# Kernel optimization log

Hardware: AMD Instinct MI355X
Metric: run time of the kernel (lower is better)

## Reference

```python
import jax, jax.numpy as jnp
import numpy as np

D_MODEL = 1024
N_HEADS = 16
HEAD_DIM = D_MODEL // N_HEADS
BATCH = 4
SEQ = 2048


def setup_inputs() -> dict:
    key = jax.random.key(0)
    ks = jax.random.split(key, 5)
    # Xavier uniform bound for square d_model x d_model weights
    bound = np.sqrt(6.0 / (D_MODEL + D_MODEL))
    x = jax.random.normal(ks[0], (BATCH, SEQ, D_MODEL), dtype=jnp.float32)
    attention_mask = jnp.ones((BATCH, SEQ), dtype=jnp.int32)
    wq = jax.random.uniform(ks[1], (D_MODEL, D_MODEL), jnp.float32, -bound, bound)
    wk = jax.random.uniform(ks[2], (D_MODEL, D_MODEL), jnp.float32, -bound, bound)
    wv = jax.random.uniform(ks[3], (D_MODEL, D_MODEL), jnp.float32, -bound, bound)
    wo = jax.random.uniform(ks[4], (D_MODEL, D_MODEL), jnp.float32, -bound, bound)
    return {"x": x, "attention_mask": attention_mask,
            "wq": wq, "wk": wk, "wv": wv, "wo": wo}


def reference(x, attention_mask, wq, wk, wv, wo):
    # x: (B, S, D). Linear weights stored torch-style (out, in): y = x @ W^T
    B, S, D = x.shape
    H, Hd = N_HEADS, HEAD_DIM
    scale = np.sqrt(Hd).astype(np.float32)

    def split_heads(t):  # (B,S,D) -> (B,H,S,Hd)
        return t.reshape(B, S, H, Hd).transpose(0, 2, 1, 3)

    q = split_heads(jnp.einsum('bsd,ed->bse', x, wq))
    k = split_heads(jnp.einsum('bsd,ed->bse', x, wk))
    v = split_heads(jnp.einsum('bsd,ed->bse', x, wv))

    scores = jnp.einsum('bhqd,bhkd->bhqk', q, k) / scale  # (B,H,S,S)

    causal = jnp.tril(jnp.ones((S, S), dtype=bool))  # True = keep
    keep = causal[None, None, :, :] & (attention_mask[:, None, None, :] != 0)
    scores = jnp.where(keep, scores, -jnp.inf)

    attn = jax.nn.softmax(scores, axis=-1)  # dropout: eval mode (identity)
    out = jnp.einsum('bhqk,bhkd->bhqd', attn, v)  # (B,H,S,Hd)
    out = out.transpose(0, 2, 1, 3).reshape(B, S, D)
    return jnp.einsum('bsd,ed->bse', out, wo)
```

## Files before the change

kernel.cpp:

```cpp
#include <hip/hip_runtime.h>
#include <cstdint>
#include <cstddef>

#define D_MODEL 1024
#define N_HEADS 16
#define HEAD_DIM 64
#define BATCH 4
#define SEQ 2048
#define M_TOTAL (BATCH * SEQ)

typedef __attribute__((ext_vector_type(8))) short bf16x8;
typedef __attribute__((ext_vector_type(4))) float f32x4;
typedef __attribute__((ext_vector_type(16))) float f32x16;

#define Q_SCALE 0.18033688011112042f

__device__ __forceinline__ unsigned short f2bu(float f) {
    union { float f; unsigned u; } x; x.f = f;
    unsigned r = x.u + 0x7FFFu + ((x.u >> 16) & 1u);
    return (unsigned short)(r >> 16);
}
__device__ __forceinline__ unsigned short f2bu_fast(float f) {
    union { float f; unsigned u; } x; x.f = f;
    return (unsigned short)((x.u + 0x8000u) >> 16);
}

__device__ __forceinline__ void async16(void* lds, const void* g) {
    __builtin_amdgcn_global_load_lds(
        (const __attribute__((address_space(1))) void*)g,
        (__attribute__((address_space(3))) void*)lds, 16, 0, 0);
}

__global__ __launch_bounds__(256) void cast_all(const float* __restrict__ x,
                                                const float* __restrict__ wq,
                                                const float* __restrict__ wk,
                                                const float* __restrict__ wv,
                                                const float* __restrict__ wo,
                                                unsigned short* __restrict__ dst) {
    const size_t NE = (size_t)M_TOTAL * D_MODEL;
    const size_t WE = (size_t)D_MODEL * D_MODEL;
    size_t i4 = (size_t)blockIdx.x * 256 + threadIdx.x;
    size_t e = i4 * 4;
    const float* src; size_t off;
    if (e < NE) { src = x; off = e; }
    else {
        size_t t = e - NE;
        int r = (int)(t / WE); off = t - (size_t)r * WE;
        src = (r == 0) ? wq : (r == 1) ? wk : (r == 2) ? wv : wo;
    }
    float4 v = *(const float4*)(src + off);
    ushort4 o;
    o.x = f2bu(v.x); o.y = f2bu(v.y); o.z = f2bu(v.z); o.w = f2bu(v.w);
    ((ushort4*)dst)[i4] = o;
}

__global__ __launch_bounds__(256) void qkv_gemm(const unsigned short* __restrict__ X,
                                                const unsigned short* __restrict__ W0,
                                                const unsigned short* __restrict__ W1,
                                                const unsigned short* __restrict__ W2,
                                                unsigned short* __restrict__ Y0,
                                                unsigned short* __restrict__ Y1,
                                                unsigned short* __restrict__ Vt) {
    __shared__ short As[128 * 32];
    __shared__ short Bs[128 * 32];

    const int sel = blockIdx.x >> 3;
    const unsigned short* W = (sel == 0) ? W0 : (sel == 1) ? W1 : W2;
    const float scl = (sel == 0) ? Q_SCALE : 1.0f;

    const int tid = threadIdx.x;
    const int w = tid >> 6, lane = tid & 63, quad = lane >> 4, l15 = lane & 15;
    const int wm = w & 1, wn = w >> 1;
    const int rowBase = blockIdx.y * 128;
    const int colBase = (blockIdx.x & 7) * 128;

    f32x4 acc[4][4];
#pragma unroll
    for (int mi = 0; mi < 4; ++mi)
#pragma unroll
        for (int ni = 0; ni < 4; ++ni)
#pragma unroll
            for (int e = 0; e < 4; ++e) acc[mi][ni][e] = 0.f;

    for (int k0 = 0; k0 < 1024; k0 += 32) {
        __syncthreads();
#pragma unroll
        for (int l = 0; l < 2; ++l) {
            int c = tid + l * 256;
            int row = c >> 2, ccs = c & 3;
            int cc = ccs ^ ((row >> 1) & 3);
            async16((char*)As + c * 16, X + (size_t)(rowBase + row) * 1024 + k0 + cc * 8);
            async16((char*)Bs + c * 16, W + (size_t)(colBase + row) * 1024 + k0 + cc * 8);
        }
        __syncthreads();

        bf16x8 a[4], b[4];
#pragma unroll
        for (int mi = 0; mi < 4; ++mi) {
            int r = wm * 64 + mi * 16 + l15;
            int slot = quad ^ ((r >> 1) & 3);
            a[mi] = *(const bf16x8*)&As[r * 32 + slot * 8];
        }
#pragma unroll
        for (int ni = 0; ni < 4; ++ni) {
            int r = wn * 64 + ni * 16 + l15;
            int slot = quad ^ ((r >> 1) & 3);
            b[ni] = *(const bf16x8*)&Bs[r * 32 + slot * 8];
        }
#pragma unroll
        for (int mi = 0; mi < 4; ++mi)
#pragma unroll
            for (int ni = 0; ni < 4; ++ni)
                acc[mi][ni] = __builtin_amdgcn_mfma_f32_16x16x32_bf16(a[mi], b[ni], acc[mi][ni], 0, 0, 0);
    }

    if (sel != 2) {
        unsigned short* Y = (sel == 0) ? Y0 : Y1;
#pragma unroll
        for (int mi = 0; mi < 4; ++mi)
#pragma unroll
            for (int ni = 0; ni < 4; ++ni)
#pragma unroll
                for (int reg = 0; reg < 4; ++reg) {
                    int row = rowBase + wm * 64 + mi * 16 + quad * 4 + reg;
                    int col = colBase + wn * 64 + ni * 16 + l15;
                    Y[(size_t)row * 1024 + col] = f2bu(acc[mi][ni][reg] * scl);
                }
    } else {
#pragma unroll
        for (int mi = 0; mi < 4; ++mi) {
            int row0 = rowBase + wm * 64 + mi * 16 + quad * 4;
            int bb = row0 >> 11;
            int s0 = row0 & 2047;
#pragma unroll
            for (int ni = 0; ni < 4; ++ni) {
                int col = colBase + wn * 64 + ni * 16 + l15;
                int hh = col >> 6, dd = col & 63;
                ushort4 pk;
                pk.x = f2bu(acc[mi][ni][0]); pk.y = f2bu(acc[mi][ni][1]);
                pk.z = f2bu(acc[mi][ni][2]); pk.w = f2bu(acc[mi][ni][3]);
                *(ushort4*)(Vt + (((size_t)bb * 16 + hh) * 64 + dd) * SEQ + s0) = pk;
            }
        }
    }
}

__global__ __launch_bounds__(256) void out_gemm(const unsigned short* __restrict__ X,
                                                const unsigned short* __restrict__ W,
                                                float* __restrict__ Y) {
    __shared__ short As[128 * 32];
    __shared__ short Bs[128 * 32];

    const int tid = threadIdx.x;
    const int w = tid >> 6, lane = tid & 63, quad = lane >> 4, l15 = lane & 15;
    const int wm = w & 1, wn = w >> 1;
    const int rowBase = blockIdx.y * 128;
    const int colBase = blockIdx.x * 128;

    f32x4 acc[4][4];
#pragma unroll
    for (int mi = 0; mi < 4; ++mi)
#pragma unroll
        for (int ni = 0; ni < 4; ++ni)
#pragma unroll
            for (int e = 0; e < 4; ++e) acc[mi][ni][e] = 0.f;

    for (int k0 = 0; k0 < 1024; k0 += 32) {
        __syncthreads();
#pragma unroll
        for (int l = 0; l < 2; ++l) {
            int c = tid + l * 256;
            int row = c >> 2, ccs = c & 3;
            int cc = ccs ^ ((row >> 1) & 3);
            async16((char*)As + c * 16, X + (size_t)(rowBase + row) * 1024 + k0 + cc * 8);
            async16((char*)Bs + c * 16, W + (size_t)(colBase + row) * 1024 + k0 + cc * 8);
        }
        __syncthreads();

        bf16x8 a[4], b[4];
#pragma unroll
        for (int mi = 0; mi < 4; ++mi) {
            int r = wm * 64 + mi * 16 + l15;
            int slot = quad ^ ((r >> 1) & 3);
            a[mi] = *(const bf16x8*)&As[r * 32 + slot * 8];
        }
#pragma unroll
        for (int ni = 0; ni < 4; ++ni) {
            int r = wn * 64 + ni * 16 + l15;
            int slot = quad ^ ((r >> 1) & 3);
            b[ni] = *(const bf16x8*)&Bs[r * 32 + slot * 8];
        }
#pragma unroll
        for (int mi = 0; mi < 4; ++mi)
#pragma unroll
            for (int ni = 0; ni < 4; ++ni)
                acc[mi][ni] = __builtin_amdgcn_mfma_f32_16x16x32_bf16(a[mi], b[ni], acc[mi][ni], 0, 0, 0);
    }

#pragma unroll
    for (int mi = 0; mi < 4; ++mi)
#pragma unroll
        for (int ni = 0; ni < 4; ++ni)
#pragma unroll
            for (int reg = 0; reg < 4; ++reg) {
                int row = rowBase + wm * 64 + mi * 16 + quad * 4 + reg;
                int col = colBase + wn * 64 + ni * 16 + l15;
                Y[(size_t)row * 1024 + col] = acc[mi][ni][reg];
            }
}

__global__ __launch_bounds__(256) void flash32(const unsigned short* __restrict__ Q,
                                               const unsigned short* __restrict__ K,
                                               const unsigned short* __restrict__ Vt,
                                               const int* __restrict__ mask,
                                               unsigned short* __restrict__ CTX) {
    __shared__ short lds[9216];
    __shared__ float biasS[64];
    __shared__ int allokS;

    short* Ks = lds;
    short* Vs = lds + 4096;

    const int pid = blockIdx.x;
    const int bh = blockIdx.y;
    const int b = bh >> 4;
    const int tid = threadIdx.x;
    const int w = tid >> 6, lane = tid & 63, l31 = lane & 31, lane5 = lane >> 5;

    const size_t qkBase = (size_t)b * SEQ * D_MODEL + (size_t)(bh & 15) * HEAD_DIM;
    const size_t vtBase = (size_t)bh * HEAD_DIM * SEQ;

    int stp[2], stcc[2], stj[2];
#pragma unroll
    for (int l = 0; l < 2; ++l) {
        int c = tid + l * 256;
        int p = c >> 3, sl = c & 7;
        stp[l] = p;
        stcc[l] = sl ^ (p & 7);
        stj[l] = (p & 0x33) | ((p & 4) << 1) | ((p & 8) >> 1);
    }

    for (int phase = 0; phase < 2; ++phase) {
        const int qt = phase ? pid : 15 - pid;
        const int q0 = qt * 128;
        const int iq = q0 + w * 32 + l31;

        bf16x8 qf[4];
#pragma unroll
        for (int ks = 0; ks < 4; ++ks)
            qf[ks] = *(const bf16x8*)(Q + qkBase + (size_t)iq * D_MODEL + ks * 16 + lane5 * 8);

        float mv = -INFINITY, lv = 0.f;
        f32x16 Ot[2];
#pragma unroll
        for (int dt = 0; dt < 2; ++dt)
#pragma unroll
            for (int e = 0; e < 16; ++e) Ot[dt][e] = 0.f;

        const int ktmax = 2 * qt + 1;

        uint4 kreg[2], vreg[2];
        int mreg;
        {
            const int k0 = 0;
#pragma unroll
            for (int l = 0; l < 2; ++l) {
                kreg[l] = *(const uint4*)(K + qkBase + (size_t)(k0 + stj[l]) * D_MODEL + stcc[l] * 8);
                vreg[l] = *(const uint4*)(Vt + vtBase + (size_t)stp[l] * SEQ + k0 + stcc[l] * 8);
            }
            mreg = (tid < 64) ? mask[b * SEQ + k0 + tid] : 1;
        }

        for (int kt = 0; kt <= ktmax; ++kt) {
            const int k0 = kt * 64;
            __syncthreads();
#pragma unroll
            for (int l = 0; l < 2; ++l) {
                int c = tid + l * 256;
                *(uint4*)((char*)Ks + c * 16) = kreg[l];
                *(uint4*)((char*)Vs + c * 16) = vreg[l];
            }
            if (tid < 64) {
                biasS[tid] = mreg ? 0.f : -INFINITY;
                unsigned long long bal = __ballot(mreg != 0);
                if (tid == 0) allokS = (bal == ~0ull) ? 1 : 0;
            }
            if (kt < ktmax) {
                const int kn = k0 + 64;
#pragma unroll
                for (int l = 0; l < 2; ++l) {
                    kreg[l] = *(const uint4*)(K + qkBase + (size_t)(kn + stj[l]) * D_MODEL + stcc[l] * 8);
                    vreg[l] = *(const uint4*)(Vt + vtBase + (size_t)stp[l] * SEQ + kn + stcc[l] * 8);
                }
                mreg = (tid < 64) ? mask[b * SEQ + kn + tid] : 1;
            }
            __syncthreads();

            if (64 * kt > q0 + 32 * w + 31) continue;

            f32x16 St[2];
#pragma unroll
            for (int T = 0; T < 2; ++T)
#pragma unroll
                for (int e = 0; e < 16; ++e) St[T][e] = 0.f;
#pragma unroll
            for (int T = 0; T < 2; ++T)
#pragma unroll
                for (int ks = 0; ks < 4; ++ks) {
                    int p = T * 32 + l31;
                    int slot = (ks * 2 + lane5) ^ (p & 7);
                    bf16x8 a = *(const bf16x8*)&Ks[p * 64 + slot * 8];
                    St[T] = __builtin_amdgcn_mfma_f32_32x32x16_bf16(a, qf[ks], St[T], 0, 0, 0);
                }

            const bool partial = (k0 + 63 > q0 + 32 * w);
            if (partial) {
#pragma unroll
                for (int T = 0; T < 2; ++T)
#pragma unroll
                    for (int r = 0; r < 16; ++r) {
                        int j = k0 + 32 * T + 16 * (r >> 3) + 8 * lane5 + (r & 7);
                        if (j > iq) St[T][r] = -INFINITY;
                    }
            }
            if (!allokS) {
#pragma unroll
                for (int T = 0; T < 2; ++T)
#pragma unroll
                    for (int r = 0; r < 16; ++r)
                        St[T][r] += biasS[32 * T + 16 * (r >> 3) + 8 * lane5 + (r & 7)];
            }

            float rm = -INFINITY;
#pragma unroll
            for (int T = 0; T < 2; ++T)
#pragma unroll
                for (int r = 0; r < 16; ++r) rm = fmaxf(rm, St[T][r]);
            rm = fmaxf(rm, __shfl_xor(rm, 32));
            float mn = fmaxf(mv, rm);
            float al = (mv > -INFINITY) ? exp2f(mv - mn) : 0.f;
            float rs = 0.f;
#pragma unroll
            for (int T = 0; T < 2; ++T)
#pragma unroll
                for (int r = 0; r < 16; ++r) {
                    float pv = (St[T][r] > -INFINITY) ? exp2f(St[T][r] - mn) : 0.f;
                    St[T][r] = pv;
                    rs += pv;
                }
            rs += __shfl_xor(rs, 32);
            lv = lv * al + rs;
            mv = mn;
#pragma unroll
            for (int dt = 0; dt < 2; ++dt)
#pragma unroll
                for (int e = 0; e < 16; ++e) Ot[dt][e] *= al;

            bf16x8 pf[4];
#pragma unroll
            for (int t = 0; t < 4; ++t) {
                int T = t >> 1, hb = t & 1;
#pragma unroll
                for (int jj = 0; jj < 8; ++jj)
                    pf[t][jj] = (short)f2bu_fast(St[T][hb * 8 + jj]);
            }

#pragma unroll
            for (int dt = 0; dt < 2; ++dt)
#pragma unroll
                for (int t = 0; t < 4; ++t) {
                    int p = dt * 32 + l31;
                    int slot = (t * 2 + lane5) ^ (p & 7);
                    bf16x8 a = *(const bf16x8*)&Vs[p * 64 + slot * 8];
                    Ot[dt] = __builtin_amdgcn_mfma_f32_32x32x16_bf16(a, pf[t], Ot[dt], 0, 0, 0);
                }
        }

        __syncthreads();
        const float inv = 1.f / lv;
#pragma unroll
        for (int dt = 0; dt < 2; ++dt)
#pragma unroll
            for (int k = 0; k < 8; ++k) {
                int r0 = 2 * k;
                int d = (r0 & 3) + 4 * lane5 + 8 * (r0 >> 2) + 32 * dt;
                unsigned lo = f2bu(Ot[dt][r0] * inv);
                unsigned hi = f2bu(Ot[dt][r0 + 1] * inv);
                *(unsigned*)&lds[(w * 32 + l31) * 72 + d] = lo | (hi << 16);
            }
        __syncthreads();
#pragma unroll
        for (int k = 0; k < 4; ++k) {
            int id = tid + k * 256;
            int r = id >> 3, cc = id & 7;
            uint4 v = *(const uint4*)&lds[r * 72 + cc * 8];
            *(uint4*)(CTX + qkBase + (size_t)(q0 + r) * D_MODEL + cc * 8) = v;
        }
    }
}

extern "C" void kernel_launch(void* const* d_in, const int* in_sizes, int n_in,
                              void* d_out, int out_size, void* d_ws, size_t ws_size,
                              hipStream_t stream) {
    const float* x  = (const float*)d_in[0];
    const int* mask = (const int*)d_in[1];
    const float* wq = (const float*)d_in[2];
    const float* wk = (const float*)d_in[3];
    const float* wv = (const float*)d_in[4];
    const float* wo = (const float*)d_in[5];
    float* out = (float*)d_out;

    const size_t NE = (size_t)M_TOTAL * D_MODEL;
    const size_t WE = (size_t)D_MODEL * D_MODEL;
    unsigned short* ws  = (unsigned short*)d_ws;
    unsigned short* xb  = ws;
    unsigned short* wqb = xb + NE;
    unsigned short* wkb = wqb + WE;
    unsigned short* wvb = wkb + WE;
    unsigned short* wob = wvb + WE;
    unsigned short* Qb  = wob + WE;
    unsigned short* Kb  = Qb + NE;
    unsigned short* Vtb = Kb + NE;
    unsigned short* CTX = Vtb + NE;

    cast_all<<<(int)((NE + 4 * WE) / 4 / 256), 256, 0, stream>>>(x, wq, wk, wv, wo, ws);

    qkv_gemm<<<dim3(24, M_TOTAL / 128), 256, 0, stream>>>(xb, wqb, wkb, wvb, Qb, Kb, Vtb);

    flash32<<<dim3(8, BATCH * N_HEADS), 256, 0, stream>>>(Qb, Kb, Vtb, mask, CTX);

    out_gemm<<<dim3(D_MODEL / 128, M_TOTAL / 128), 256, 0, stream>>>(CTX, wob, out);
}
```

Measured before the change: 315.6 us.

## Skip per-tile mask work, lazily rescale softmax, use packed bf16 cvt and setprio

Each block now checks the whole padding mask once up front and skips the per-tile mask loads, ballots and bias adds when every key is valid. The online softmax only rescales O and l when the running max rises by more than 8 (log2 units), which removes most rescale multiplies. The exp2 guards are dropped and the per-element bf16 packing is replaced with hardware v_cvt_pk_bf16_f32. MFMA sections are wrapped in s_setprio. Risks: the lazy rescale lets P values reach up to 2^8 before conversion to bf16, and the extra full-mask scan adds a prologue pass per block.

After: 309.3 us. 2.0% less time.

```diff
diff --git a/kernel.cpp b/kernel.cpp
--- a/kernel.cpp
+++ b/kernel.cpp
@@ -19,10 +19,6 @@
     union { float f; unsigned u; } x; x.f = f;
     unsigned r = x.u + 0x7FFFu + ((x.u >> 16) & 1u);
     return (unsigned short)(r >> 16);
-}
-__device__ __forceinline__ unsigned short f2bu_fast(float f) {
-    union { float f; unsigned u; } x; x.f = f;
-    return (unsigned short)((x.u + 0x8000u) >> 16);
 }
 
 __device__ __forceinline__ void async16(void* lds, const void* g) {
@@ -217,6 +213,7 @@
     __shared__ short lds[9216];
     __shared__ float biasS[64];
     __shared__ int allokS;
+    __shared__ int okW[4];
 
     short* Ks = lds;
     short* Vs = lds + 4096;
@@ -229,6 +226,15 @@
 
     const size_t qkBase = (size_t)b * SEQ * D_MODEL + (size_t)(bh & 15) * HEAD_DIM;
     const size_t vtBase = (size_t)bh * HEAD_DIM * SEQ;
+
+    {
+        int ok = 1;
+        for (int i = tid; i < SEQ; i += 256) ok &= (mask[b * SEQ + i] != 0);
+        unsigned long long bal = __ballot(ok != 0);
+        if (lane == 0) okW[w] = (bal == ~0ull) ? 1 : 0;
+    }
+    __syncthreads();
+    const int allSeq = okW[0] & okW[1] & okW[2] & okW[3];
 
     int stp[2], stcc[2], stj[2];
 #pragma unroll
@@ -260,7 +266,7 @@
         const int ktmax = 2 * qt + 1;
 
         uint4 kreg[2], vreg[2];
-        int mreg;
+        int mreg = 1;
         {
             const int k0 = 0;
 #pragma unroll
@@ -268,7 +274,7 @@
                 kreg[l] = *(const uint4*)(K + qkBase + (size_t)(k0 + stj[l]) * D_MODEL + stcc[l] * 8);
                 vreg[l] = *(const uint4*)(Vt + vtBase + (size_t)stp[l] * SEQ + k0 + stcc[l] * 8);
             }
-            mreg = (tid < 64) ? mask[b * SEQ + k0 + tid] : 1;
+            if (!allSeq && tid < 64) mreg = mask[b * SEQ + k0 + tid];
         }
 
         for (int kt = 0; kt <= ktmax; ++kt) {
@@ -280,7 +286,7 @@
                 *(uint4*)((char*)Ks + c * 16) = kreg[l];
                 *(uint4*)((char*)Vs + c * 16) = vreg[l];
             }
-            if (tid < 64) {
+            if (!allSeq && tid < 64) {
                 biasS[tid] = mreg ? 0.f : -INFINITY;
                 unsigned long long bal = __ballot(mreg != 0);
                 if (tid == 0) allokS = (bal == ~0ull) ? 1 : 0;
@@ -292,7 +298,7 @@
                     kreg[l] = *(const uint4*)(K + qkBase + (size_t)(kn + stj[l]) * D_MODEL + stcc[l] * 8);
                     vreg[l] = *(const uint4*)(Vt + vtBase + (size_t)stp[l] * SEQ + kn + stcc[l] * 8);
                 }
-                mreg = (tid < 64) ? mask[b * SEQ + kn + tid] : 1;
+                if (!allSeq && tid < 64) mreg = mask[b * SEQ + kn + tid];
             }
             __syncthreads();
 
@@ -303,6 +309,7 @@
             for (int T = 0; T < 2; ++T)
 #pragma unroll
                 for (int e = 0; e < 16; ++e) St[T][e] = 0.f;
+            __builtin_amdgcn_s_setprio(1);
 #pragma unroll
             for (int T = 0; T < 2; ++T)
 #pragma unroll
@@ -312,6 +319,7 @@
                     bf16x8 a = *(const bf16x8*)&Ks[p * 64 + slot * 8];
                     St[T] = __builtin_amdgcn_mfma_f32_32x32x16_bf16(a, qf[ks], St[T], 0, 0, 0);
                 }
+            __builtin_amdgcn_s_setprio(0);
 
             const bool partial = (k0 + 63 > q0 + 32 * w);
             if (partial) {
@@ -323,7 +331,7 @@
                         if (j > iq) St[T][r] = -INFINITY;
                     }
             }
-            if (!allokS) {
+            if (!allSeq && !allokS) {
 #pragma unroll
                 for (int T = 0; T < 2; ++T)
 #pragma unroll
@@ -338,33 +346,46 @@
                 for (int r = 0; r < 16; ++r) rm = fmaxf(rm, St[T][r]);
             rm = fmaxf(rm, __shfl_xor(rm, 32));
             float mn = fmaxf(mv, rm);
-            float al = (mv > -INFINITY) ? exp2f(mv - mn) : 0.f;
+            if (mn > mv + 8.f) {
+                float al = exp2f(mv - mn);
+                lv *= al;
+#pragma unroll
+                for (int dt = 0; dt < 2; ++dt)
+#pragma unroll
+                    for (int e = 0; e < 16; ++e) Ot[dt][e] *= al;
+                mv = mn;
+            }
             float rs = 0.f;
 #pragma unroll
             for (int T = 0; T < 2; ++T)
 #pragma unroll
                 for (int r = 0; r < 16; ++r) {
-                    float pv = (St[T][r] > -INFINITY) ? exp2f(St[T][r] - mn) : 0.f;
+                    float pv = exp2f(St[T][r] - mv);
                     St[T][r] = pv;
                     rs += pv;
                 }
             rs += __shfl_xor(rs, 32);
-            lv = lv * al + rs;
-            mv = mn;
-#pragma unroll
-            for (int dt = 0; dt < 2; ++dt)
-#pragma unroll
-                for (int e = 0; e < 16; ++e) Ot[dt][e] *= al;
+            lv += rs;
 
             bf16x8 pf[4];
 #pragma unroll
             for (int t = 0; t < 4; ++t) {
-                int T = t >> 1, hb = t & 1;
-#pragma unroll
-                for (int jj = 0; jj < 8; ++jj)
-                    pf[t][jj] = (short)f2bu_fast(St[T][hb * 8 + jj]);
-            }
-
+                const int T = t >> 1, hb = t & 1;
+                unsigned u0, u1, u2, u3;
+                asm("v_cvt_pk_bf16_f32 %0, %1, %2" : "=v"(u0)
+                    : "v"(St[T][hb * 8 + 0]), "v"(St[T][hb * 8 + 1]));
+                asm("v_cvt_pk_bf16_f32 %0, %1, %2" : "=v"(u1)
+                    : "v"(St[T][hb * 8 + 2]), "v"(St[T][hb * 8 + 3]));
+                asm("v_cvt_pk_bf16_f32 %0, %1, %2" : "=v"(u2)
+                    : "v"(St[T][hb * 8 + 4]), "v"(St[T][hb * 8 + 5]));
+                asm("v_cvt_pk_bf16_f32 %0, %1, %2" : "=v"(u3)
+                    : "v"(St[T][hb * 8 + 6]), "v"(St[T][hb * 8 + 7]));
+                union { unsigned u[4]; bf16x8 v; } pk;
+                pk.u[0] = u0; pk.u[1] = u1; pk.u[2] = u2; pk.u[3] = u3;
+                pf[t] = pk.v;
+            }
+
+            __builtin_amdgcn_s_setprio(1);
 #pragma unroll
             for (int dt = 0; dt < 2; ++dt)
 #pragma unroll
@@ -374,6 +395,7 @@
                     bf16x8 a = *(const bf16x8*)&Vs[p * 64 + slot * 8];
                     Ot[dt] = __builtin_amdgcn_mfma_f32_32x32x16_bf16(a, pf[t], Ot[dt], 0, 0, 0);
                 }
+            __builtin_amdgcn_s_setprio(0);
         }
 
         __syncthreads();
```
